# Optimization experiments

Measured on AMD Instinct MI355X. Metric: run time of the kernel, lower is better.

Reference implementation:

```python
import jax, jax.numpy as jnp
import numpy as np

D_MODEL = 1024
H = 16
D_K = D_MODEL // H
NEG = -1000000000.0


def setup_inputs() -> dict:
    key = jax.random.key(0)
    ks = jax.random.split(key, 12)
    B, S, D = 2, 2048, D_MODEL
    scale = 1.0 / np.sqrt(D)
    inp = {
        "q": jax.random.normal(ks[0], (B, S, D), jnp.float32),
        "k": jax.random.normal(ks[1], (B, S, D), jnp.float32),
        "v": jax.random.normal(ks[2], (B, S, D), jnp.float32),
        "mask": jnp.tril(jnp.ones((S, S), bool))[None, None],  # causal (1,1,S,S)
        "Wq": jax.random.normal(ks[3], (D, D), jnp.float32) * scale,
        "bq": jax.random.normal(ks[4], (D,), jnp.float32) * scale,
        "Wk": jax.random.normal(ks[5], (D, D), jnp.float32) * scale,
        "bk": jax.random.normal(ks[6], (D,), jnp.float32) * scale,
        "Wv": jax.random.normal(ks[7], (D, D), jnp.float32) * scale,
        "bv": jax.random.normal(ks[8], (D,), jnp.float32) * scale,
        "Wo": jax.random.normal(ks[9], (D, D), jnp.float32) * scale,
        "bo": jax.random.normal(ks[10], (D,), jnp.float32) * scale,
    }
    return inp


def _split_heads(x):
    B, S, _ = x.shape
    return x.reshape(B, S, H, D_K).transpose(0, 2, 1, 3)  # (B,H,S,dk)


def reference(q, k, v, mask, Wq, bq, Wk, bk, Wv, bv, Wo, bo):
    # nn.Linear: x @ W.T + b
    query = _split_heads(q @ Wq.T + bq)
    key_ = _split_heads(k @ Wk.T + bk)
    value = _split_heads(v @ Wv.T + bv)
    scores = jnp.einsum("bhqd,bhkd->bhqk", query, key_) / jnp.sqrt(
        jnp.asarray(D_K, jnp.float32)
    )
    scores = jnp.where(mask, scores, NEG)  # masked_fill(mask==0, -1e9)
    attn = jax.nn.softmax(scores, axis=-1)  # dropout p=0 -> identity
    x = jnp.einsum("bhqk,bhkd->bhqd", attn, value)
    B, _, S, _ = x.shape
    x = x.transpose(0, 2, 1, 3).reshape(B, S, D_MODEL)
    return x @ Wo.T + bo
```

## Files before the change

### kernel.cpp

```cpp
#include <hip/hip_runtime.h>
#include <stdint.h>

typedef unsigned short ushort_t;
typedef __attribute__((ext_vector_type(8))) __bf16 bf16x8;
typedef __attribute__((ext_vector_type(4))) float f32x4;
typedef __attribute__((ext_vector_type(4))) unsigned int uint32x4;

__device__ __forceinline__ ushort_t f2bf(float f) {
  unsigned u = __float_as_uint(f);
  u += 0x7FFFu + ((u >> 16) & 1u);
  return (ushort_t)(u >> 16);
}

__device__ __forceinline__ unsigned cvt_pk_bf16(float lo, float hi) {
  unsigned r;
  asm("v_cvt_pk_bf16_f32 %0, %1, %2" : "=v"(r) : "v"(lo), "v"(hi));
  return r;
}

__device__ __forceinline__ float exp2_fast(float x) {
  float r;
  asm("v_exp_f32 %0, %1" : "=v"(r) : "v"(x));
  return r;
}

__device__ __forceinline__ uint32x4 ld8_f32(const float* p) {
  f32x4 a = *(const f32x4*)p;
  f32x4 b = *(const f32x4*)(p + 4);
  uint32x4 r;
  r.x = (unsigned)f2bf(a[0]) | ((unsigned)f2bf(a[1]) << 16);
  r.y = (unsigned)f2bf(a[2]) | ((unsigned)f2bf(a[3]) << 16);
  r.z = (unsigned)f2bf(b[0]) | ((unsigned)f2bf(b[1]) << 16);
  r.w = (unsigned)f2bf(b[2]) | ((unsigned)f2bf(b[3]) << 16);
  return r;
}
__device__ __forceinline__ uint32x4 ld8_bf16(const ushort_t* p) {
  return *(const uint32x4*)p;
}

__device__ __forceinline__ void gll16(const void* g, void* l) {
  __builtin_amdgcn_global_load_lds((const __attribute__((address_space(1))) void*)g,
                                   (__attribute__((address_space(3))) void*)l,
                                   16, 0, 0);
}

struct CvtArgs {
  const float* src[7];
  ushort_t* dst[7];
  int cnt[7];
};
__global__ void cvt_multi(CvtArgs a) {
  const int seg = blockIdx.y;
  const int idx = (blockIdx.x * 256 + threadIdx.x) * 8;
  if (idx < a.cnt[seg])
    *(uint32x4*)(a.dst[seg] + idx) = ld8_f32(a.src[seg] + idx);
}

template<bool A_F32, bool B_F32>
__device__ __forceinline__ void gemm_tile_reg(const void* __restrict__ Ablk_,
                                              const void* __restrict__ Wblk_,
                                              ushort_t* As, ushort_t* Bs,
                                              const int K, const int w, const int l,
                                              f32x4 acc[4][4])
{
  const float*    Af = (const float*)Ablk_;
  const ushort_t* Ab = (const ushort_t*)Ablk_;
  const float*    Wf = (const float*)Wblk_;
  const ushort_t* Wb = (const ushort_t*)Wblk_;
  const int sr = l >> 2, sk = (l & 3) << 3;
  const int lr = l & 15, q4 = l >> 4;
  const int wrow = (w >> 1) << 6, wcol = (w & 1) << 6;

  for (int k0 = 0; k0 < K; k0 += 32) {
    uint32x4 ra[2], rb[2];
#pragma unroll
    for (int cc = 0; cc < 2; ++cc) {
      const int ch  = cc * 4 + w;
      const int row = ch * 16 + sr;
      ra[cc] = A_F32 ? ld8_f32(Af + (size_t)row * K + k0 + sk)
                     : ld8_bf16(Ab + (size_t)row * K + k0 + sk);
      rb[cc] = B_F32 ? ld8_f32(Wf + (size_t)row * K + k0 + sk)
                     : ld8_bf16(Wb + (size_t)row * K + k0 + sk);
    }
    __syncthreads();
#pragma unroll
    for (int cc = 0; cc < 2; ++cc) {
      const int ch = cc * 4 + w;
      *(uint32x4*)(As + ch * 512 + l * 8) = ra[cc];
      *(uint32x4*)(Bs + ch * 512 + l * 8) = rb[cc];
    }
    __syncthreads();
    bf16x8 a[4], b[4];
#pragma unroll
    for (int i = 0; i < 4; ++i)
      a[i] = *(const bf16x8*)(As + (wrow + i * 16 + lr) * 32 + q4 * 8);
#pragma unroll
    for (int j = 0; j < 4; ++j)
      b[j] = *(const bf16x8*)(Bs + (wcol + j * 16 + lr) * 32 + q4 * 8);
#pragma unroll
    for (int i = 0; i < 4; ++i)
#pragma unroll
      for (int j = 0; j < 4; ++j)
        acc[i][j] = __builtin_amdgcn_mfma_f32_16x16x32_bf16(a[i], b[j], acc[i][j], 0, 0, 0);
  }
}

__device__ __forceinline__ void proj_epilogue(int z, f32x4 acc[4][4], const float* bias,
                                              ushort_t* O, int bm, int bn, int w, int l)
{
  const int lr = l & 15, q4 = l >> 4;
  const int wrow = (w >> 1) << 6, wcol = (w & 1) << 6;
  if (z == 2) {
#pragma unroll
    for (int i = 0; i < 4; ++i) {
      const int r0 = bm * 128 + wrow + i * 16 + q4 * 4;
      const int b_ = r0 >> 11, s_ = r0 & 2047;
#pragma unroll
      for (int j = 0; j < 4; ++j) {
        const int c = bn * 128 + wcol + j * 16 + lr;
        const float bb = bias[c];
        const int hb = b_ * 16 + (c >> 6);
        const int d_ = c & 63;
        ushort4 pk;
        pk.x = f2bf(acc[i][j][0] + bb);
        pk.y = f2bf(acc[i][j][1] + bb);
        pk.z = f2bf(acc[i][j][2] + bb);
        pk.w = f2bf(acc[i][j][3] + bb);
        *(ushort4*)(O + ((size_t)hb * 64 + d_) * 2048 + s_) = pk;
      }
    }
  } else {
#pragma unroll
    for (int i = 0; i < 4; ++i) {
#pragma unroll
      for (int j = 0; j < 4; ++j) {
        const int c = bn * 128 + wcol + j * 16 + lr;
        const float bb = bias[c];
        const int h_ = c >> 6, d_ = c & 63;
#pragma unroll
        for (int rg = 0; rg < 4; ++rg) {
          const int r = bm * 128 + wrow + i * 16 + q4 * 4 + rg;
          const int b_ = r >> 11, s_ = r & 2047;
          O[((size_t)(b_ * 16 + h_) * 2048 + s_) * 64 + d_] = f2bf(acc[i][j][rg] + bb);
        }
      }
    }
  }
}

__device__ __forceinline__ void out_epilogue(f32x4 acc[4][4], const float* bo,
                                             float* out, int bm, int bn, int w, int l)
{
  const int lr = l & 15, q4 = l >> 4;
  const int wrow = (w >> 1) << 6, wcol = (w & 1) << 6;
#pragma unroll
  for (int i = 0; i < 4; ++i) {
#pragma unroll
    for (int j = 0; j < 4; ++j) {
      const int c = bn * 128 + wcol + j * 16 + lr;
      const float bb = bo[c];
#pragma unroll
      for (int rg = 0; rg < 4; ++rg) {
        const int r = bm * 128 + wrow + i * 16 + q4 * 4 + rg;
        out[(size_t)r * 1024 + c] = acc[i][j][rg] + bb;
      }
    }
  }
}

__device__ __forceinline__ int swz_off(int r, int cc) {
  return (r * 4 + (cc ^ ((r >> 1) & 3))) * 8;
}

__launch_bounds__(256, 3)
__global__ void proj_qkv_p3(const ushort_t* __restrict__ qb, const ushort_t* __restrict__ kb,
                            const ushort_t* __restrict__ vb,
                            const ushort_t* __restrict__ Wqb, const ushort_t* __restrict__ Wkb,
                            const ushort_t* __restrict__ Wvb,
                            const float* __restrict__ bq, const float* __restrict__ bk,
                            const float* __restrict__ bv,
                            ushort_t* __restrict__ Qo, ushort_t* __restrict__ Ko,
                            ushort_t* __restrict__ Vo)
{
  const int z = blockIdx.z;
  const ushort_t* A = (z == 0) ? qb : (z == 1) ? kb : vb;
  const ushort_t* W = (z == 0) ? Wqb : (z == 1) ? Wkb : Wvb;
  const float* bias = (z == 0) ? bq : (z == 1) ? bk : bv;
  ushort_t* O       = (z == 0) ? Qo : (z == 1) ? Ko : Vo;

  const int K = 1024;
  const int NT = 32;
  const int bm = blockIdx.x, bn = blockIdx.y;
  const int tid = threadIdx.x;
  const int w = tid >> 6, l = tid & 63;
  const int lr = l & 15, q4 = l >> 4;

  __shared__ ushort_t lds[3 * 8192];

  const ushort_t* Ablk = A + (size_t)(bm * 128) * K;
  const ushort_t* Wblk = W + (size_t)(bn * 128) * K;

  size_t so_[2];
  int ldA_[2], ldB_[2];
#pragma unroll
  for (int i = 0; i < 2; ++i) {
    const int p = i * 256 + tid;
    const int r = p >> 2;
    const int cc = (p & 3) ^ ((r >> 1) & 3);
    so_[i]  = (size_t)r * K + cc * 8;
    ldA_[i] = p * 8;
    ldB_[i] = 4096 + p * 8;
  }

  int aoff[4], boff[4];
#pragma unroll
  for (int mf = 0; mf < 4; ++mf) aoff[mf] = swz_off((w >> 1) * 64 + mf * 16 + lr, q4);
#pragma unroll
  for (int nf = 0; nf < 4; ++nf) boff[nf] = 4096 + swz_off((w & 1) * 64 + nf * 16 + lr, q4);

#pragma unroll
  for (int tt = 0; tt < 2; ++tt) {
    ushort_t* buf = lds + tt * 8192;
    gll16(Ablk + so_[0] + tt * 32, buf + ldA_[0]);
    gll16(Ablk + so_[1] + tt * 32, buf + ldA_[1]);
    gll16(Wblk + so_[0] + tt * 32, buf + ldB_[0]);
    gll16(Wblk + so_[1] + tt * 32, buf + ldB_[1]);
  }
  asm volatile("s_waitcnt vmcnt(4)" ::: "memory");
  __builtin_amdgcn_s_barrier();

  f32x4 acc[4][4];
#pragma unroll
  for (int i = 0; i < 4; ++i)
#pragma unroll
    for (int j = 0; j < 4; ++j) acc[i][j] = (f32x4)0.0f;

  int rbi = 0, sbi = 2;
  for (int t_ = 0; t_ < NT; ++t_) {
    const ushort_t* rb = lds + rbi * 8192;
    bf16x8 Af[4], Bf[4];
#pragma unroll
    for (int mf = 0; mf < 4; ++mf) Af[mf] = *(const bf16x8*)(rb + aoff[mf]);
#pragma unroll
    for (int nf = 0; nf < 4; ++nf) Bf[nf] = *(const bf16x8*)(rb + boff[nf]);

    if (t_ + 2 < NT) {
      ushort_t* sb = lds + sbi * 8192;
      const int kel = (t_ + 2) * 32;
      gll16(Ablk + so_[0] + kel, sb + ldA_[0]);
      gll16(Ablk + so_[1] + kel, sb + ldA_[1]);
      gll16(Wblk + so_[0] + kel, sb + ldB_[0]);
      gll16(Wblk + so_[1] + kel, sb + ldB_[1]);
    }

    __builtin_amdgcn_s_setprio(1);
#pragma unroll
    for (int mf = 0; mf < 4; ++mf)
#pragma unroll
      for (int nf = 0; nf < 4; ++nf)
        acc[mf][nf] = __builtin_amdgcn_mfma_f32_16x16x32_bf16(Af[mf], Bf[nf], acc[mf][nf], 0, 0, 0);
    __builtin_amdgcn_s_setprio(0);

    if (t_ < NT - 2)       asm volatile("s_waitcnt vmcnt(4)" ::: "memory");
    else if (t_ == NT - 2) asm volatile("s_waitcnt vmcnt(0)" ::: "memory");
    __builtin_amdgcn_s_barrier();

    rbi = (rbi == 2) ? 0 : rbi + 1;
    sbi = (sbi == 2) ? 0 : sbi + 1;
  }

  proj_epilogue(z, acc, bias, O, bm, bn, w, l);
}

__launch_bounds__(256, 2)
__global__ void proj_qkv_f32(const float* __restrict__ qi, const float* __restrict__ ki,
                             const float* __restrict__ vi,
                             const float* __restrict__ Wq, const float* __restrict__ Wk,
                             const float* __restrict__ Wv,
                             const float* __restrict__ bq, const float* __restrict__ bk,
                             const float* __restrict__ bv,
                             ushort_t* __restrict__ Qo, ushort_t* __restrict__ Ko,
                             ushort_t* __restrict__ Vo)
{
  const int z = blockIdx.z;
  const float* A    = (z == 0) ? qi : (z == 1) ? ki : vi;
  const float* W    = (z == 0) ? Wq : (z == 1) ? Wk : Wv;
  const float* bias = (z == 0) ? bq : (z == 1) ? bk : bv;
  ushort_t* O       = (z == 0) ? Qo : (z == 1) ? Ko : Vo;
  const int K = 1024;
  const int bm = blockIdx.y, bn = blockIdx.x;
  const int t = threadIdx.x, w = t >> 6, l = t & 63;
  __shared__ ushort_t As[128 * 32];
  __shared__ ushort_t Bs[128 * 32];
  f32x4 acc[4][4];
#pragma unroll
  for (int i = 0; i < 4; ++i)
#pragma unroll
    for (int j = 0; j < 4; ++j) acc[i][j] = (f32x4)0.0f;
  gemm_tile_reg<true, true>(A + (size_t)(bm * 128) * K, W + (size_t)(bn * 128) * K,
                            As, Bs, K, w, l, acc);
  proj_epilogue(z, acc, bias, O, bm, bn, w, l);
}

#define PPAD 72
__launch_bounds__(256, 4)
__global__ void attn(const ushort_t* __restrict__ Qh, const ushort_t* __restrict__ Kh,
                     const ushort_t* __restrict__ Vh, ushort_t* __restrict__ X)
{
  const int S = 2048;
  const int id = blockIdx.x;
  const int hb = (id & 7) * 4 + ((id >> 3) & 3);
  const int j = id >> 5;
  const int qt = (j < 8) ? (31 - j) : (j < 16) ? (j - 8) : (j < 24) ? (39 - j) : (j - 16);
  const int q0 = qt * 64;

  __shared__ ushort_t Ks[64 * 64];
  __shared__ ushort_t Vt[64 * 64];
  __shared__ ushort_t Ps[4 * 16 * PPAD];

  const int t = threadIdx.x, w = t >> 6, l = t & 63;
  const int lr = l & 15, q4 = l >> 4;

  const ushort_t* Qbase = Qh + (size_t)hb * S * 64;
  const ushort_t* Kbase = Kh + (size_t)hb * S * 64;
  const ushort_t* Vbase = Vh + (size_t)hb * 64 * S;

  bf16x8 qa[2];
#pragma unroll
  for (int ks = 0; ks < 2; ++ks)
    qa[ks] = *(const bf16x8*)(Qbase + (size_t)(q0 + w * 16 + lr) * 64 + ks * 32 + q4 * 8);

  f32x4 o_acc[4];
#pragma unroll
  for (int jj = 0; jj < 4; ++jj) o_acc[jj] = (f32x4)0.0f;
  float lsum = 0.0f;

  const int nkt = qt + 1;
  const int strow = l >> 3;
  const int stcol = (l & 7) * 8;
  const int swcol = ((l & 7) ^ strow) * 8;
  const int qi = q0 + w * 16 + lr;

  int koff[2][4], voff[2][4];
#pragma unroll
  for (int ks = 0; ks < 2; ++ks)
#pragma unroll
    for (int f = 0; f < 4; ++f) {
      const int row = f * 16 + lr;
      const int slot = ((ks * 4 + q4) ^ (lr & 7)) * 8;
      koff[ks][f] = row * 64 + slot;
      voff[ks][f] = row * 64 + slot;
    }

  const float C1 = 0.125f * 1.44269504f;
  const float C0 = -12.0f * 1.44269504f;

  uint32x4 kreg[2], vreg[2];
#pragma unroll
  for (int cc = 0; cc < 2; ++cc) {
    const int row = (cc * 4 + w) * 8 + strow;
    kreg[cc] = *(const uint32x4*)(Kbase + (size_t)row * 64 + stcol);
    vreg[cc] = *(const uint32x4*)(Vbase + (size_t)row * S + stcol);
  }

  for (int kt = 0; kt < nkt; ++kt) {
    __syncthreads();
#pragma unroll
    for (int cc = 0; cc < 2; ++cc) {
      const int row = (cc * 4 + w) * 8 + strow;
      *(uint32x4*)(Ks + row * 64 + swcol) = kreg[cc];
      *(uint32x4*)(Vt + row * 64 + swcol) = vreg[cc];
    }
    __syncthreads();

    const int ktn = (kt + 1 < nkt) ? kt + 1 : kt;
#pragma unroll
    for (int cc = 0; cc < 2; ++cc) {
      const int row = (cc * 4 + w) * 8 + strow;
      kreg[cc] = *(const uint32x4*)(Kbase + (size_t)(ktn * 64 + row) * 64 + stcol);
      vreg[cc] = *(const uint32x4*)(Vbase + (size_t)row * S + ktn * 64 + stcol);
    }

    f32x4 s_acc[4];
#pragma unroll
    for (int jj = 0; jj < 4; ++jj) s_acc[jj] = (f32x4)0.0f;
#pragma unroll
    for (int ks = 0; ks < 2; ++ks)
#pragma unroll
      for (int nf = 0; nf < 4; ++nf) {
        bf16x8 kb = *(const bf16x8*)(Ks + koff[ks][nf]);
        s_acc[nf] = __builtin_amdgcn_mfma_f32_16x16x32_bf16(kb, qa[ks], s_acc[nf], 0, 0, 0);
      }

    const bool need_mask = (kt == qt);
#pragma unroll
    for (int nf = 0; nf < 4; ++nf)
#pragma unroll
      for (int rg = 0; rg < 4; ++rg) {
        const int kvi = kt * 64 + nf * 16 + q4 * 4 + rg;
        float p = exp2_fast(__builtin_fmaf(s_acc[nf][rg], C1, C0));
        if (need_mask && kvi > qi) p = 0.0f;
        s_acc[nf][rg] = p;
        lsum += p;
      }

    ushort_t* Pw = Ps + w * (16 * PPAD);
#pragma unroll
    for (int nf = 0; nf < 4; ++nf) {
      uint2 pk2;
      pk2.x = cvt_pk_bf16(s_acc[nf][0], s_acc[nf][1]);
      pk2.y = cvt_pk_bf16(s_acc[nf][2], s_acc[nf][3]);
      *(uint2*)(Pw + lr * PPAD + nf * 16 + q4 * 4) = pk2;
    }

    __asm__ volatile("s_waitcnt lgkmcnt(0)" ::: "memory");

#pragma unroll
    for (int ks = 0; ks < 2; ++ks) {
      bf16x8 pb = *(const bf16x8*)(Pw + lr * PPAD + ks * 32 + q4 * 8);
#pragma unroll
      for (int df = 0; df < 4; ++df) {
        bf16x8 vb = *(const bf16x8*)(Vt + voff[ks][df]);
        o_acc[df] = __builtin_amdgcn_mfma_f32_16x16x32_bf16(vb, pb, o_acc[df], 0, 0, 0);
      }
    }
  }

  const int b_ = hb >> 4, h_ = hb & 15;
  float s = lsum;
  s += __shfl_xor(s, 16);
  s += __shfl_xor(s, 32);
  const float inv = 1.0f / s;
  const int r = q0 + w * 16 + lr;
  ushort_t* Xrow = X + ((size_t)b_ * 2048 + r) * 1024 + h_ * 64;
#pragma unroll
  for (int df = 0; df < 4; ++df) {
    uint2 st;
    st.x = cvt_pk_bf16(o_acc[df][0] * inv, o_acc[df][1] * inv);
    st.y = cvt_pk_bf16(o_acc[df][2] * inv, o_acc[df][3] * inv);
    *(uint2*)(Xrow + df * 16 + q4 * 4) = st;
  }
}

__launch_bounds__(256, 2)
__global__ void out_gemm_p2(const ushort_t* __restrict__ Xin, const ushort_t* __restrict__ Wob,
                            const float* __restrict__ bo, float* __restrict__ out)
{
  const int K = 1024;
  const int NT = 32;
  const int bm = blockIdx.x, bn = blockIdx.y;
  const int tid = threadIdx.x;
  const int w = tid >> 6, l = tid & 63;
  const int lr = l & 15, q4 = l >> 4;
  const int wm = w >> 1, wn = w & 1;

  __shared__ ushort_t lds[3 * 6144];

  const ushort_t* Ablk = Xin + (size_t)(bm * 128) * K;
  const ushort_t* Wblk = Wob + (size_t)(bn * 64) * K;

  size_t soA[2], soB;
  int ldA[2], ldB;
#pragma unroll
  for (int i = 0; i < 2; ++i) {
    const int p = i * 256 + tid;
    const int r = p >> 2;
    const int cc = (p & 3) ^ ((r >> 1) & 3);
    soA[i] = (size_t)r * K + cc * 8;
    ldA[i] = p * 8;
  }
  {
    const int p = tid;
    const int r = p >> 2;
    const int cc = (p & 3) ^ ((r >> 1) & 3);
    soB = (size_t)r * K + cc * 8;
    ldB = 4096 + p * 8;
  }

  int aoff[4], boff[2];
#pragma unroll
  for (int mf = 0; mf < 4; ++mf) aoff[mf] = swz_off(wm * 64 + mf * 16 + lr, q4);
#pragma unroll
  for (int nf = 0; nf < 2; ++nf) boff[nf] = 4096 + swz_off(wn * 32 + nf * 16 + lr, q4);

#pragma unroll
  for (int tt = 0; tt < 2; ++tt) {
    ushort_t* buf = lds + tt * 6144;
    gll16(Ablk + soA[0] + tt * 32, buf + ldA[0]);
    gll16(Ablk + soA[1] + tt * 32, buf + ldA[1]);
    gll16(Wblk + soB + tt * 32, buf + ldB);
  }
  asm volatile("s_waitcnt vmcnt(3)" ::: "memory");
  __builtin_amdgcn_s_barrier();

  f32x4 acc[4][2];
#pragma unroll
  for (int i = 0; i < 4; ++i)
#pragma unroll
    for (int jj = 0; jj < 2; ++jj) acc[i][jj] = (f32x4)0.0f;

  int rbi = 0, sbi = 2;
  for (int t_ = 0; t_ < NT; ++t_) {
    const ushort_t* rb = lds + rbi * 6144;
    bf16x8 Af[4], Bf[2];
#pragma unroll
    for (int mf = 0; mf < 4; ++mf) Af[mf] = *(const bf16x8*)(rb + aoff[mf]);
#pragma unroll
    for (int nf = 0; nf < 2; ++nf) Bf[nf] = *(const bf16x8*)(rb + boff[nf]);

    if (t_ + 2 < NT) {
      ushort_t* sb = lds + sbi * 6144;
      const int kel = (t_ + 2) * 32;
      gll16(Ablk + soA[0] + kel, sb + ldA[0]);
      gll16(Ablk + soA[1] + kel, sb + ldA[1]);
      gll16(Wblk + soB + kel, sb + ldB);
    }

    __builtin_amdgcn_s_setprio(1);
#pragma unroll
    for (int mf = 0; mf < 4; ++mf)
#pragma unroll
      for (int nf = 0; nf < 2; ++nf)
        acc[mf][nf] = __builtin_amdgcn_mfma_f32_16x16x32_bf16(Af[mf], Bf[nf], acc[mf][nf], 0, 0, 0);
    __builtin_amdgcn_s_setprio(0);

    if (t_ < NT - 2)       asm volatile("s_waitcnt vmcnt(3)" ::: "memory");
    else if (t_ == NT - 2) asm volatile("s_waitcnt vmcnt(0)" ::: "memory");
    __builtin_amdgcn_s_barrier();

    rbi = (rbi == 2) ? 0 : rbi + 1;
    sbi = (sbi == 2) ? 0 : sbi + 1;
  }

#pragma unroll
  for (int mf = 0; mf < 4; ++mf) {
#pragma unroll
    for (int nf = 0; nf < 2; ++nf) {
      const int c = bn * 64 + wn * 32 + nf * 16 + lr;
      const float bb = bo[c];
#pragma unroll
      for (int rg = 0; rg < 4; ++rg) {
        const int r = bm * 128 + wm * 64 + mf * 16 + q4 * 4 + rg;
        out[(size_t)r * 1024 + c] = acc[mf][nf][rg] + bb;
      }
    }
  }
}

__launch_bounds__(256, 2)
__global__ void out_gemm_f32(const ushort_t* __restrict__ Xin, const float* __restrict__ Wo,
                             const float* __restrict__ bo, float* __restrict__ out)
{
  const int K = 1024;
  const int bm = blockIdx.y, bn = blockIdx.x;
  const int t = threadIdx.x, w = t >> 6, l = t & 63;
  __shared__ ushort_t As[128 * 32];
  __shared__ ushort_t Bs[128 * 32];
  f32x4 acc[4][4];
#pragma unroll
  for (int i = 0; i < 4; ++i)
#pragma unroll
    for (int j = 0; j < 4; ++j) acc[i][j] = (f32x4)0.0f;
  gemm_tile_reg<false, true>(Xin + (size_t)(bm * 128) * K, Wo + (size_t)(bn * 128) * K,
                             As, Bs, K, w, l, acc);
  out_epilogue(acc, bo, out, bm, bn, w, l);
}

extern "C" void kernel_launch(void* const* d_in, const int* in_sizes, int n_in,
                              void* d_out, int out_size, void* d_ws, size_t ws_size,
                              hipStream_t stream) {
  (void)in_sizes; (void)n_in; (void)out_size;
  const float* q  = (const float*)d_in[0];
  const float* k  = (const float*)d_in[1];
  const float* v  = (const float*)d_in[2];
  const float* Wq = (const float*)d_in[4];
  const float* bq = (const float*)d_in[5];
  const float* Wk = (const float*)d_in[6];
  const float* bk = (const float*)d_in[7];
  const float* Wv = (const float*)d_in[8];
  const float* bv = (const float*)d_in[9];
  const float* Wo = (const float*)d_in[10];
  const float* bo = (const float*)d_in[11];

  ushort_t* ws = (ushort_t*)d_ws;
  const size_t SEG = (size_t)2 * 2048 * 1024;
  const size_t WSEG = (size_t)1024 * 1024;
  const size_t NEED = (3 * SEG + 4 * WSEG + 2 * SEG) * sizeof(ushort_t);

  if (ws_size >= NEED) {
    ushort_t* qb  = ws;
    ushort_t* kb  = qb + SEG;
    ushort_t* vb  = kb + SEG;
    ushort_t* Wqb = vb + SEG;
    ushort_t* Wkb = Wqb + WSEG;
    ushort_t* Wvb = Wkb + WSEG;
    ushort_t* Wob = Wvb + WSEG;
    ushort_t* Qh  = Wob + WSEG;
    ushort_t* Kh  = Qh + SEG;
    ushort_t* X   = qb;
    ushort_t* Vh  = (ushort_t*)d_out;

    CvtArgs ca;
    ca.src[0] = q;  ca.dst[0] = qb;  ca.cnt[0] = (int)SEG;
    ca.src[1] = k;  ca.dst[1] = kb;  ca.cnt[1] = (int)SEG;
    ca.src[2] = v;  ca.dst[2] = vb;  ca.cnt[2] = (int)SEG;
    ca.src[3] = Wq; ca.dst[3] = Wqb; ca.cnt[3] = (int)WSEG;
    ca.src[4] = Wk; ca.dst[4] = Wkb; ca.cnt[4] = (int)WSEG;
    ca.src[5] = Wv; ca.dst[5] = Wvb; ca.cnt[5] = (int)WSEG;
    ca.src[6] = Wo; ca.dst[6] = Wob; ca.cnt[6] = (int)WSEG;
    cvt_multi<<<dim3(2048, 7), 256, 0, stream>>>(ca);

    proj_qkv_p3<<<dim3(32, 8, 3), 256, 0, stream>>>(qb, kb, vb, Wqb, Wkb, Wvb,
                                                    bq, bk, bv, Qh, Kh, Vh);
    attn<<<dim3(1024), 256, 0, stream>>>(Qh, Kh, Vh, X);
    out_gemm_p2<<<dim3(32, 16), 256, 0, stream>>>(X, Wob, bo, (float*)d_out);
  } else {
    ushort_t* Qh = ws;
    ushort_t* Kh = Qh + SEG;
    ushort_t* X  = Kh + SEG;
    ushort_t* Vh = (ushort_t*)d_out;
    proj_qkv_f32<<<dim3(8, 32, 3), 256, 0, stream>>>(q, k, v, Wq, Wk, Wv,
                                                     bq, bk, bv, Qh, Kh, Vh);
    attn<<<dim3(1024), 256, 0, stream>>>(Qh, Kh, Vh, X);
    out_gemm_f32<<<dim3(8, 32), 256, 0, stream>>>(X, Wo, bo, (float*)d_out);
  }
}
```

Measured before the change: 204.8 us.

## Double-buffer K/V tiles in LDS with two-deep register prefetch in attention

Turns the attention loop's single LDS K/V buffer into two ping-ponged buffers, with two register sets prefetching tiles two iterations ahead. This cuts the per-iteration barriers from two to one and lets global loads overlap more compute. The P scratch tile switches from padding to an XOR swizzle, which frees LDS for the second buffer. In exchange it uses more registers and LDS, relies on hand-written vmcnt waits that must match the order loads are issued, and may lower occupancy.

```diff
diff --git a/kernel.cpp b/kernel.cpp
--- a/kernel.cpp
+++ b/kernel.cpp
@@ -302,7 +302,6 @@
   proj_epilogue(z, acc, bias, O, bm, bn, w, l);
 }
 
-#define PPAD 72
 __launch_bounds__(256, 4)
 __global__ void attn(const ushort_t* __restrict__ Qh, const ushort_t* __restrict__ Kh,
                      const ushort_t* __restrict__ Vh, ushort_t* __restrict__ X)
@@ -314,9 +313,9 @@
   const int qt = (j < 8) ? (31 - j) : (j < 16) ? (j - 8) : (j < 24) ? (39 - j) : (j - 16);
   const int q0 = qt * 64;
 
-  __shared__ ushort_t Ks[64 * 64];
-  __shared__ ushort_t Vt[64 * 64];
-  __shared__ ushort_t Ps[4 * 16 * PPAD];
+  __shared__ ushort_t Ks[2][64 * 64];
+  __shared__ ushort_t Vt[2][64 * 64];
+  __shared__ ushort_t Ps[4 * 16 * 64];
 
   const int t = threadIdx.x, w = t >> 6, l = t & 63;
   const int lr = l & 15, q4 = l >> 4;
@@ -341,45 +340,58 @@
   const int swcol = ((l & 7) ^ strow) * 8;
   const int qi = q0 + w * 16 + lr;
 
-  int koff[2][4], voff[2][4];
+  int koff[2][4];
 #pragma unroll
   for (int ks = 0; ks < 2; ++ks)
 #pragma unroll
     for (int f = 0; f < 4; ++f) {
       const int row = f * 16 + lr;
-      const int slot = ((ks * 4 + q4) ^ (lr & 7)) * 8;
-      koff[ks][f] = row * 64 + slot;
-      voff[ks][f] = row * 64 + slot;
-    }
+      koff[ks][f] = row * 64 + ((ks * 4 + q4) ^ (lr & 7)) * 8;
+    }
+
+  int poffw[4], poffr[2];
+#pragma unroll
+  for (int nf = 0; nf < 4; ++nf)
+    poffw[nf] = lr * 64 + (((nf * 2 + (q4 >> 1)) ^ (lr & 7)) * 8) + (q4 & 1) * 4;
+#pragma unroll
+  for (int ks = 0; ks < 2; ++ks)
+    poffr[ks] = lr * 64 + (((ks * 4 + q4) ^ (lr & 7)) * 8);
 
   const float C1 = 0.125f * 1.44269504f;
   const float C0 = -12.0f * 1.44269504f;
 
-  uint32x4 kreg[2], vreg[2];
-#pragma unroll
-  for (int cc = 0; cc < 2; ++cc) {
-    const int row = (cc * 4 + w) * 8 + strow;
-    kreg[cc] = *(const uint32x4*)(Kbase + (size_t)row * 64 + stcol);
-    vreg[cc] = *(const uint32x4*)(Vbase + (size_t)row * S + stcol);
+  uint32x4 kA[2], vA[2], kB[2], vB[2];
+  const int r0s = w * 8 + strow;
+  const int r1s = (4 + w) * 8 + strow;
+
+  {
+    const int t1 = (nkt > 1) ? 1 : 0;
+    kA[0] = *(const uint32x4*)(Kbase + (size_t)r0s * 64 + stcol);
+    kA[1] = *(const uint32x4*)(Kbase + (size_t)r1s * 64 + stcol);
+    vA[0] = *(const uint32x4*)(Vbase + (size_t)r0s * S + stcol);
+    vA[1] = *(const uint32x4*)(Vbase + (size_t)r1s * S + stcol);
+    kB[0] = *(const uint32x4*)(Kbase + (size_t)(t1 * 64 + r0s) * 64 + stcol);
+    kB[1] = *(const uint32x4*)(Kbase + (size_t)(t1 * 64 + r1s) * 64 + stcol);
+    vB[0] = *(const uint32x4*)(Vbase + (size_t)r0s * S + t1 * 64 + stcol);
+    vB[1] = *(const uint32x4*)(Vbase + (size_t)r1s * S + t1 * 64 + stcol);
+    asm volatile("s_waitcnt vmcnt(4)" ::: "memory");
+    *(uint32x4*)(&Ks[0][0] + r0s * 64 + swcol) = kA[0];
+    *(uint32x4*)(&Ks[0][0] + r1s * 64 + swcol) = kA[1];
+    *(uint32x4*)(&Vt[0][0] + r0s * 64 + swcol) = vA[0];
+    *(uint32x4*)(&Vt[0][0] + r1s * 64 + swcol) = vA[1];
+    const int t2 = (nkt > 2) ? 2 : nkt - 1;
+    kA[0] = *(const uint32x4*)(Kbase + (size_t)(t2 * 64 + r0s) * 64 + stcol);
+    kA[1] = *(const uint32x4*)(Kbase + (size_t)(t2 * 64 + r1s) * 64 + stcol);
+    vA[0] = *(const uint32x4*)(Vbase + (size_t)r0s * S + t2 * 64 + stcol);
+    vA[1] = *(const uint32x4*)(Vbase + (size_t)r1s * S + t2 * 64 + stcol);
+    asm volatile("s_waitcnt lgkmcnt(0)" ::: "memory");
+    __builtin_amdgcn_s_barrier();
   }
 
   for (int kt = 0; kt < nkt; ++kt) {
-    __syncthreads();
-#pragma unroll
-    for (int cc = 0; cc < 2; ++cc) {
-      const int row = (cc * 4 + w) * 8 + strow;
-      *(uint32x4*)(Ks + row * 64 + swcol) = kreg[cc];
-      *(uint32x4*)(Vt + row * 64 + swcol) = vreg[cc];
-    }
-    __syncthreads();
-
-    const int ktn = (kt + 1 < nkt) ? kt + 1 : kt;
-#pragma unroll
-    for (int cc = 0; cc < 2; ++cc) {
-      const int row = (cc * 4 + w) * 8 + strow;
-      kreg[cc] = *(const uint32x4*)(Kbase + (size_t)(ktn * 64 + row) * 64 + stcol);
-      vreg[cc] = *(const uint32x4*)(Vbase + (size_t)row * S + ktn * 64 + stcol);
-    }
+    const int p = kt & 1;
+    const ushort_t* Kp = &Ks[p][0];
+    const ushort_t* Vp = &Vt[p][0];
 
     f32x4 s_acc[4];
 #pragma unroll
@@ -388,7 +400,7 @@
     for (int ks = 0; ks < 2; ++ks)
 #pragma unroll
       for (int nf = 0; nf < 4; ++nf) {
-        bf16x8 kb = *(const bf16x8*)(Ks + koff[ks][nf]);
+        bf16x8 kb = *(const bf16x8*)(Kp + koff[ks][nf]);
         s_acc[nf] = __builtin_amdgcn_mfma_f32_16x16x32_bf16(kb, qa[ks], s_acc[nf], 0, 0, 0);
       }
 
@@ -398,32 +410,58 @@
 #pragma unroll
       for (int rg = 0; rg < 4; ++rg) {
         const int kvi = kt * 64 + nf * 16 + q4 * 4 + rg;
-        float p = exp2_fast(__builtin_fmaf(s_acc[nf][rg], C1, C0));
-        if (need_mask && kvi > qi) p = 0.0f;
-        s_acc[nf][rg] = p;
-        lsum += p;
-      }
-
-    ushort_t* Pw = Ps + w * (16 * PPAD);
+        float pv = exp2_fast(__builtin_fmaf(s_acc[nf][rg], C1, C0));
+        if (need_mask && kvi > qi) pv = 0.0f;
+        s_acc[nf][rg] = pv;
+        lsum += pv;
+      }
+
+    ushort_t* Pw = Ps + w * (16 * 64);
 #pragma unroll
     for (int nf = 0; nf < 4; ++nf) {
       uint2 pk2;
       pk2.x = cvt_pk_bf16(s_acc[nf][0], s_acc[nf][1]);
       pk2.y = cvt_pk_bf16(s_acc[nf][2], s_acc[nf][3]);
-      *(uint2*)(Pw + lr * PPAD + nf * 16 + q4 * 4) = pk2;
+      *(uint2*)(Pw + poffw[nf]) = pk2;
     }
 
     __asm__ volatile("s_waitcnt lgkmcnt(0)" ::: "memory");
 
 #pragma unroll
     for (int ks = 0; ks < 2; ++ks) {
-      bf16x8 pb = *(const bf16x8*)(Pw + lr * PPAD + ks * 32 + q4 * 8);
+      bf16x8 pb = *(const bf16x8*)(Pw + poffr[ks]);
 #pragma unroll
       for (int df = 0; df < 4; ++df) {
-        bf16x8 vb = *(const bf16x8*)(Vt + voff[ks][df]);
+        bf16x8 vb = *(const bf16x8*)(Vp + koff[ks][df]);
         o_acc[df] = __builtin_amdgcn_mfma_f32_16x16x32_bf16(vb, pb, o_acc[df], 0, 0, 0);
       }
     }
+
+    if (kt + 1 < nkt) {
+      asm volatile("s_waitcnt vmcnt(4)" ::: "memory");
+      const int nt3 = (kt + 3 < nkt) ? kt + 3 : nkt - 1;
+      if (p == 0) {
+        *(uint32x4*)(&Ks[1][0] + r0s * 64 + swcol) = kB[0];
+        *(uint32x4*)(&Ks[1][0] + r1s * 64 + swcol) = kB[1];
+        *(uint32x4*)(&Vt[1][0] + r0s * 64 + swcol) = vB[0];
+        *(uint32x4*)(&Vt[1][0] + r1s * 64 + swcol) = vB[1];
+        kB[0] = *(const uint32x4*)(Kbase + (size_t)(nt3 * 64 + r0s) * 64 + stcol);
+        kB[1] = *(const uint32x4*)(Kbase + (size_t)(nt3 * 64 + r1s) * 64 + stcol);
+        vB[0] = *(const uint32x4*)(Vbase + (size_t)r0s * S + nt3 * 64 + stcol);
+        vB[1] = *(const uint32x4*)(Vbase + (size_t)r1s * S + nt3 * 64 + stcol);
+      } else {
+        *(uint32x4*)(&Ks[0][0] + r0s * 64 + swcol) = kA[0];
+        *(uint32x4*)(&Ks[0][0] + r1s * 64 + swcol) = kA[1];
+        *(uint32x4*)(&Vt[0][0] + r0s * 64 + swcol) = vA[0];
+        *(uint32x4*)(&Vt[0][0] + r1s * 64 + swcol) = vA[1];
+        kA[0] = *(const uint32x4*)(Kbase + (size_t)(nt3 * 64 + r0s) * 64 + stcol);
+        kA[1] = *(const uint32x4*)(Kbase + (size_t)(nt3 * 64 + r1s) * 64 + stcol);
+        vA[0] = *(const uint32x4*)(Vbase + (size_t)r0s * S + nt3 * 64 + stcol);
+        vA[1] = *(const uint32x4*)(Vbase + (size_t)r1s * S + nt3 * 64 + stcol);
+      }
+    }
+    asm volatile("s_waitcnt lgkmcnt(0)" ::: "memory");
+    __builtin_amdgcn_s_barrier();
   }
 
   const int b_ = hb >> 4, h_ = hb & 15;
```

After: 210.9 us. +3.0%, slower.
